# Kernel optimization log

Measured on AMD Instinct MI355X. Metric: run time of the kernel, lower is better.

The kernel has to match this reference:

```python
import jax, jax.numpy as jnp
import numpy as np

EDGE = 255                      # env_edge_size
ADD = (EDGE - 1) // 2           # additional_size = 127
AX = EDGE + ADD                 # axial_size = 382 (input height H)
BATCH = 16
CHAN = 32


def setup_inputs() -> dict:
    key = jax.random.key(0)
    k1, k2 = jax.random.split(key)
    axial_tensor = jax.random.normal(k1, (BATCH, CHAN, AX, EDGE), dtype=jnp.float32)
    offset = jax.random.randint(k2, (BATCH, 2), 0, EDGE)  # (q, r) per batch
    return {"axial_tensor": axial_tensor, "offset": offset}


def reference(axial_tensor, offset):
    # Faithful translation of AxialTranslatorRotator.translate (translate=True path).
    B, C, H, W = axial_tensor.shape          # H = axial_size, W = edge_size
    add = H - W                              # additional_size
    S = 2 * H + 1                            # placeholder side = 2*axial_size + 1

    q = offset[:, 0]
    r = offset[:, 1]
    uoff = q - r // 2                        # us in torch code (floor div, r >= 0)

    # _axial_indices flatten order: loops over (u=i in [0,W), v=j in [0,H)),
    # flat index k = i*H + j; original gather reads x[b, c, j, i].
    j = jnp.arange(H)                        # v coordinate (indexes input H dim)
    i = jnp.arange(W)                        # u coordinate (indexes input W dim)

    # transformed indices: assigned_u = v - uoff + H - add ; assigned_v = u - r + H
    au = j[None, None, :] - uoff[:, None, None] + (H - add)   # (B, 1, H)
    av = i[None, :, None] - r[:, None, None] + H               # (B, W, 1)
    au = jnp.broadcast_to(au, (B, W, H)).reshape(B, W * H)
    av = jnp.broadcast_to(av, (B, W, H)).reshape(B, W * H)

    # values in matching flat order: vals[b, i*H + j, c] = x[b, c, j, i]
    vals = jnp.transpose(axial_tensor, (0, 3, 2, 1)).reshape(B, W * H, C)

    out = jnp.zeros((B, S, S, C), dtype=axial_tensor.dtype)
    out = out.at[jnp.arange(B)[:, None], au, av].set(vals, unique_indices=True)
    out = jnp.transpose(out, (0, 3, 1, 2))   # (B, C, S, S)

    # AxialMapBounds
    u_min = H - add - uoff
    v_min = H - r
    u_max = u_min + H
    v_max = v_min + W
    return out, u_min, u_max, v_min, v_max
```

## Files before the change

### kernel.cpp

```cpp
#include <hip/hip_runtime.h>

namespace {
constexpr int kH = 382;
constexpr int kW = 255;
constexpr int kS = 765;
constexpr int kPlaneIn  = kH * kW;
constexpr int kPlaneOut = kS * kS;
constexpr int kNPlanes  = 512;
constexpr int kWavesPerPlane = 16;
constexpr int kRowsPerWave   = 24;
constexpr int kCopyBlocks = kNPlanes * kWavesPerPlane / 4;
constexpr unsigned long long kOutElems =
    (unsigned long long)kNPlanes * (unsigned long long)kPlaneOut;
typedef float floatv4 __attribute__((ext_vector_type(4)));
}

__global__ __launch_bounds__(256) void band_copy_kernel(
    const float* __restrict__ in, const int* __restrict__ off,
    float* __restrict__ out)
{
    if (blockIdx.x == (unsigned)kCopyBlocks) {
        int i = (int)threadIdx.x;
        if (i < 64) {
            int b = i & 15;
            int which = i >> 4;
            int q = off[2 * b];
            int r = off[2 * b + 1];
            int u_min = 255 - (q - (r >> 1));
            int v_min = 382 - r;
            int val = (which == 0) ? u_min
                    : (which == 1) ? (u_min + kH)
                    : (which == 2) ? v_min
                                   : (v_min + kW);
            out[kOutElems + (unsigned)i] = (float)val;
        }
        return;
    }

    const int lane = (int)threadIdx.x & 63;
    const int gw   = (int)(blockIdx.x * 4u + ((unsigned)threadIdx.x >> 6));
    const int p    = gw >> 4;
    const int sub  = gw & 15;
    const int b    = p >> 5;

    const int q   = off[2 * b];
    const int r   = off[2 * b + 1];
    const int ulo = 255 - (q - (r >> 1));
    const int vlo = 382 - r;

    const unsigned inplane = (unsigned)p * (unsigned)kPlaneIn;
    const unsigned outband = (unsigned)p * (unsigned)kPlaneOut
                           + (unsigned)ulo * (unsigned)kS + (unsigned)vlo;

    const int h0 = sub * kRowsPerWave;
    const int h1 = (h0 + kRowsPerWave < kH) ? h0 + kRowsPerWave : kH;

    for (int h = h0; h < h1; ++h) {
        const unsigned inbase = inplane + (unsigned)h * (unsigned)kW;
        const unsigned S      = outband + (unsigned)h * (unsigned)kS;

        const int pad  = (int)((0u - S) & 3u);
        const int nvec = (kW - pad) >> 2;
        const int tail = kW - pad - 4 * nvec;

        if (lane < nvec) {
            const int d = pad + 4 * lane;
            floatv4 v;
            __builtin_memcpy(&v, in + inbase + d, 16);
            __builtin_nontemporal_store(
                v, reinterpret_cast<floatv4*>(out + S + d));
        }
        if (lane < pad)
            __builtin_nontemporal_store(in[inbase + lane], out + S + lane);
        if (lane < tail) {
            const int d = pad + 4 * nvec + lane;
            __builtin_nontemporal_store(in[inbase + d], out + S + d);
        }
    }
}

extern "C" void kernel_launch(void* const* d_in, const int* in_sizes, int n_in,
                              void* d_out, int out_size, void* d_ws, size_t ws_size,
                              hipStream_t stream) {
    const float* in  = (const float*)d_in[0];
    const int*   off = (const int*)d_in[1];
    float*       out = (float*)d_out;

    hipMemsetAsync(out, 0, kOutElems * sizeof(float), stream);
    band_copy_kernel<<<dim3(kCopyBlocks + 1), dim3(256), 0, stream>>>(in, off, out);
}
```

Measured before the change: 313.1 us.

## Replace full memset with targeted zero fill and full-width band row writes

Removes the whole-output memset and instead zero-fills only the rows above and below the band with a custom kernel, while the band kernel writes complete output rows including zero padding around the copied data. Each output element is written once, removing redundant write traffic for the band region. The risk is that a hand-written fill kernel may not reach the memset's store bandwidth, and the wider rows add boundary-handling branches.

```diff
diff --git a/kernel.cpp b/kernel.cpp
--- a/kernel.cpp
+++ b/kernel.cpp
@@ -7,19 +7,57 @@
 constexpr int kPlaneIn  = kH * kW;
 constexpr int kPlaneOut = kS * kS;
 constexpr int kNPlanes  = 512;
+constexpr int kZeroSlices = 8;
 constexpr int kWavesPerPlane = 16;
 constexpr int kRowsPerWave   = 24;
-constexpr int kCopyBlocks = kNPlanes * kWavesPerPlane / 4;
+constexpr int kBandBlocks = kNPlanes * kWavesPerPlane / 4;
 constexpr unsigned long long kOutElems =
     (unsigned long long)kNPlanes * (unsigned long long)kPlaneOut;
 typedef float floatv4 __attribute__((ext_vector_type(4)));
 }
 
-__global__ __launch_bounds__(256) void band_copy_kernel(
+__global__ __launch_bounds__(256) void zero_fill_kernel(
+    const int* __restrict__ off, float* __restrict__ out)
+{
+    const int run   = (int)blockIdx.x;
+    const int p     = run >> 1;
+    const int which = run & 1;
+    const int b     = p >> 5;
+
+    const int q   = off[2 * b];
+    const int r   = off[2 * b + 1];
+    const int ulo = 255 - (q - (r >> 1));
+
+    unsigned start; int ndw;
+    if (which == 0) {
+        start = (unsigned)p * (unsigned)kPlaneOut;
+        ndw   = ulo * kS;
+    } else {
+        start = (unsigned)p * (unsigned)kPlaneOut + (unsigned)(ulo + kH) * (unsigned)kS;
+        ndw   = (383 - ulo) * kS;
+    }
+    const int pad  = (int)((0u - start) & 3u);
+    const int nvec = (ndw - pad) >> 2;
+    const int tail = ndw - pad - 4 * nvec;
+
+    const floatv4 z4 = {0.f, 0.f, 0.f, 0.f};
+    for (int i = (int)(blockIdx.y * 256u + threadIdx.x); i < nvec;
+         i += 256 * kZeroSlices) {
+        __builtin_nontemporal_store(
+            z4, reinterpret_cast<floatv4*>(out + start + pad + 4 * i));
+    }
+    if (blockIdx.y == 0) {
+        const int t = (int)threadIdx.x;
+        if (t < pad)  __builtin_nontemporal_store(0.f, out + start + t);
+        if (t < tail) __builtin_nontemporal_store(0.f, out + start + pad + 4 * nvec + t);
+    }
+}
+
+__global__ __launch_bounds__(256) void band_rows_kernel(
     const float* __restrict__ in, const int* __restrict__ off,
     float* __restrict__ out)
 {
-    if (blockIdx.x == (unsigned)kCopyBlocks) {
+    if (blockIdx.x == (unsigned)kBandBlocks) {
         int i = (int)threadIdx.x;
         if (i < 64) {
             int b = i & 15;
@@ -48,33 +86,44 @@
     const int ulo = 255 - (q - (r >> 1));
     const int vlo = 382 - r;
 
-    const unsigned inplane = (unsigned)p * (unsigned)kPlaneIn;
+    const float* __restrict__ inplane = in + (size_t)p * (size_t)kPlaneIn;
     const unsigned outband = (unsigned)p * (unsigned)kPlaneOut
-                           + (unsigned)ulo * (unsigned)kS + (unsigned)vlo;
+                           + (unsigned)ulo * (unsigned)kS;
 
     const int h0 = sub * kRowsPerWave;
     const int h1 = (h0 + kRowsPerWave < kH) ? h0 + kRowsPerWave : kH;
 
     for (int h = h0; h < h1; ++h) {
-        const unsigned inbase = inplane + (unsigned)h * (unsigned)kW;
-        const unsigned S      = outband + (unsigned)h * (unsigned)kS;
+        const float* __restrict__ inrow = inplane + (size_t)h * (size_t)kW;
+        const unsigned S = outband + (unsigned)h * (unsigned)kS;
 
         const int pad  = (int)((0u - S) & 3u);
-        const int nvec = (kW - pad) >> 2;
-        const int tail = kW - pad - 4 * nvec;
+        const int nvec = (kS - pad) >> 2;
+        const int tail = kS - pad - 4 * nvec;
 
-        if (lane < nvec) {
-            const int d = pad + 4 * lane;
-            floatv4 v;
-            __builtin_memcpy(&v, in + inbase + d, 16);
-            __builtin_nontemporal_store(
-                v, reinterpret_cast<floatv4*>(out + S + d));
-        }
-        if (lane < pad)
-            __builtin_nontemporal_store(in[inbase + lane], out + S + lane);
-        if (lane < tail) {
-            const int d = pad + 4 * nvec + lane;
-            __builtin_nontemporal_store(in[inbase + d], out + S + d);
+        if (lane < pad)  __builtin_nontemporal_store(0.f, out + S + lane);
+        if (lane < tail) __builtin_nontemporal_store(0.f, out + S + pad + 4 * nvec + lane);
+
+#pragma unroll
+        for (int j = 0; j < 3; ++j) {
+            const int fi = lane + 64 * j;
+            if (fi < nvec) {
+                const int d   = pad + 4 * fi;
+                const int rel = d - vlo;
+                floatv4 v;
+                if (rel >= 0 && rel + 3 < kW) {
+                    __builtin_memcpy(&v, inrow + rel, 16);
+                } else if (rel + 3 < 0 || rel >= kW) {
+                    v = (floatv4){0.f, 0.f, 0.f, 0.f};
+                } else {
+                    v.x = ((unsigned)(rel    ) < (unsigned)kW) ? inrow[rel]     : 0.f;
+                    v.y = ((unsigned)(rel + 1) < (unsigned)kW) ? inrow[rel + 1] : 0.f;
+                    v.z = ((unsigned)(rel + 2) < (unsigned)kW) ? inrow[rel + 2] : 0.f;
+                    v.w = ((unsigned)(rel + 3) < (unsigned)kW) ? inrow[rel + 3] : 0.f;
+                }
+                __builtin_nontemporal_store(
+                    v, reinterpret_cast<floatv4*>(out + S + d));
+            }
         }
     }
 }
@@ -86,6 +135,6 @@
     const int*   off = (const int*)d_in[1];
     float*       out = (float*)d_out;
 
-    hipMemsetAsync(out, 0, kOutElems * sizeof(float), stream);
-    band_copy_kernel<<<dim3(kCopyBlocks + 1), dim3(256), 0, stream>>>(in, off, out);
+    zero_fill_kernel<<<dim3(kNPlanes * 2, kZeroSlices), dim3(256), 0, stream>>>(off, out);
+    band_rows_kernel<<<dim3(kBandBlocks + 1), dim3(256), 0, stream>>>(in, off, out);
 }
```

New measurement: 338.3 us. 8.1% more time.
